# Performance work log

Measured on AMD Instinct MI355X. Metric: run time of the kernel, lower is better.

## Reference

```python
import jax, jax.numpy as jnp
import numpy as np

NBINS = 64
VMIN, VMAX = -3.0, 3.0  # value_range


def setup_inputs() -> dict:
    key = jax.random.key(0)
    x = jax.random.normal(key, (4096, 8192), dtype=jnp.float32)
    return {"x": x}


def reference(x):
    # input_axis = 1 (last axis): per-row fixed-width histogram, normalized by row length.
    B, N = x.shape
    # Bucketize: same semantics as tf.histogram_fixed_width -- scale into [0, nbins),
    # clip out-of-range values into the edge bins.
    scale = NBINS / (VMAX - VMIN)
    bins = jnp.clip(jnp.floor((x - VMIN) * scale).astype(jnp.int32), 0, NBINS - 1)  # [B, N]
    # Fused parallel scatter-add: offset each row into its own bin range.
    row = jnp.arange(B, dtype=jnp.int32)[:, None]               # [B, 1]
    flat_idx = (row * NBINS + bins).reshape(-1)                 # [B*N]
    counts = jax.ops.segment_sum(
        jnp.ones((B * N,), dtype=jnp.float32), flat_idx, num_segments=B * NBINS
    ).reshape(B, NBINS)
    # TF layer returns count / input.shape[input_axis]
    return counts / jnp.float32(N)
```

## Files before the change

### kernel.cpp

```cpp
#include <hip/hip_runtime.h>

#define NBINS 64
#define NCOPIES 64
#define BLOCK 256
#define UNROLL 8

__global__ __launch_bounds__(BLOCK, 8) void hist_rows_kernel(
    const float* __restrict__ x, float* __restrict__ out, int ncols) {
    __shared__ unsigned int hist[NBINS * NCOPIES];

    const int t = threadIdx.x;
    const int row = blockIdx.x;

    #pragma unroll
    for (int i = t; i < NBINS * NCOPIES; i += BLOCK) hist[i] = 0u;
    __syncthreads();

    const int copy = t & (NCOPIES - 1);
    const float vmin = -3.0f;
    const float scale = 64.0f / 6.0f;

    const float4* xr = (const float4*)(x + (size_t)row * (size_t)ncols);
    const int nvec = ncols >> 2;

    int base = 0;
    for (; base + UNROLL * BLOCK <= nvec; base += UNROLL * BLOCK) {
        float4 buf[UNROLL];
        #pragma unroll
        for (int k = 0; k < UNROLL; ++k) buf[k] = xr[base + k * BLOCK + t];
        #pragma unroll
        for (int k = 0; k < UNROLL; ++k) {
            float4 v = buf[k];
            float f0 = __builtin_amdgcn_fmed3f((v.x - vmin) * scale, 0.0f, 63.0f);
            float f1 = __builtin_amdgcn_fmed3f((v.y - vmin) * scale, 0.0f, 63.0f);
            float f2 = __builtin_amdgcn_fmed3f((v.z - vmin) * scale, 0.0f, 63.0f);
            float f3 = __builtin_amdgcn_fmed3f((v.w - vmin) * scale, 0.0f, 63.0f);
            int b0 = (int)f0, b1 = (int)f1, b2 = (int)f2, b3 = (int)f3;
            atomicAdd(&hist[b0 * NCOPIES + copy], 1u);
            atomicAdd(&hist[b1 * NCOPIES + copy], 1u);
            atomicAdd(&hist[b2 * NCOPIES + copy], 1u);
            atomicAdd(&hist[b3 * NCOPIES + copy], 1u);
        }
    }
    for (int i = base + t; i < nvec; i += BLOCK) {
        float4 v = xr[i];
        float f0 = __builtin_amdgcn_fmed3f((v.x - vmin) * scale, 0.0f, 63.0f);
        float f1 = __builtin_amdgcn_fmed3f((v.y - vmin) * scale, 0.0f, 63.0f);
        float f2 = __builtin_amdgcn_fmed3f((v.z - vmin) * scale, 0.0f, 63.0f);
        float f3 = __builtin_amdgcn_fmed3f((v.w - vmin) * scale, 0.0f, 63.0f);
        atomicAdd(&hist[(int)f0 * NCOPIES + copy], 1u);
        atomicAdd(&hist[(int)f1 * NCOPIES + copy], 1u);
        atomicAdd(&hist[(int)f2 * NCOPIES + copy], 1u);
        atomicAdd(&hist[(int)f3 * NCOPIES + copy], 1u);
    }
    __syncthreads();

    if (t < NBINS) {
        unsigned int s = 0;
        #pragma unroll
        for (int c = 0; c < NCOPIES; ++c)
            s += hist[t * NCOPIES + ((c + t) & (NCOPIES - 1))];
        const float inv = 1.0f / (float)ncols;
        out[(size_t)row * NBINS + t] = (float)s * inv;
    }
}

extern "C" void kernel_launch(void* const* d_in, const int* in_sizes, int n_in,
                              void* d_out, int out_size, void* d_ws, size_t ws_size,
                              hipStream_t stream) {
    const float* x = (const float*)d_in[0];
    float* out = (float*)d_out;
    const int nrows = out_size / NBINS;
    const int ncols = in_sizes[0] / nrows;
    hist_rows_kernel<<<nrows, BLOCK, 0, stream>>>(x, out, ncols);
}
```

Before: 184.7 us.

## Specialize single-tile row path, overlap loads with LDS clear, parallelize bin reduction

Adds a fast path for rows of exactly UNROLL*BLOCK float4 (8192 columns) that issues all global loads before zeroing the shared histogram, so memory latency overlaps the clear and barrier. The clear uses 128-bit LDS stores. The final reduction now uses all 256 threads (4 per bin, each summing 16 copies) combined via shuffles instead of 64 threads summing 64 copies. A generic fallback path also handles a scalar tail for column counts not divisible by 4, which the old code silently dropped.

```diff
diff --git a/kernel.cpp b/kernel.cpp
--- a/kernel.cpp
+++ b/kernel.cpp
@@ -11,11 +11,6 @@
 
     const int t = threadIdx.x;
     const int row = blockIdx.x;
-
-    #pragma unroll
-    for (int i = t; i < NBINS * NCOPIES; i += BLOCK) hist[i] = 0u;
-    __syncthreads();
-
     const int copy = t & (NCOPIES - 1);
     const float vmin = -3.0f;
     const float scale = 64.0f / 6.0f;
@@ -23,11 +18,17 @@
     const float4* xr = (const float4*)(x + (size_t)row * (size_t)ncols);
     const int nvec = ncols >> 2;
 
-    int base = 0;
-    for (; base + UNROLL * BLOCK <= nvec; base += UNROLL * BLOCK) {
+    if (nvec == UNROLL * BLOCK) {
         float4 buf[UNROLL];
         #pragma unroll
-        for (int k = 0; k < UNROLL; ++k) buf[k] = xr[base + k * BLOCK + t];
+        for (int k = 0; k < UNROLL; ++k) buf[k] = xr[k * BLOCK + t];
+
+        uint4* h4 = (uint4*)hist;
+        #pragma unroll
+        for (int i = t; i < (NBINS * NCOPIES) / 4; i += BLOCK)
+            h4[i] = make_uint4(0u, 0u, 0u, 0u);
+        __syncthreads();
+
         #pragma unroll
         for (int k = 0; k < UNROLL; ++k) {
             float4 v = buf[k];
@@ -41,27 +42,41 @@
             atomicAdd(&hist[b2 * NCOPIES + copy], 1u);
             atomicAdd(&hist[b3 * NCOPIES + copy], 1u);
         }
-    }
-    for (int i = base + t; i < nvec; i += BLOCK) {
-        float4 v = xr[i];
-        float f0 = __builtin_amdgcn_fmed3f((v.x - vmin) * scale, 0.0f, 63.0f);
-        float f1 = __builtin_amdgcn_fmed3f((v.y - vmin) * scale, 0.0f, 63.0f);
-        float f2 = __builtin_amdgcn_fmed3f((v.z - vmin) * scale, 0.0f, 63.0f);
-        float f3 = __builtin_amdgcn_fmed3f((v.w - vmin) * scale, 0.0f, 63.0f);
-        atomicAdd(&hist[(int)f0 * NCOPIES + copy], 1u);
-        atomicAdd(&hist[(int)f1 * NCOPIES + copy], 1u);
-        atomicAdd(&hist[(int)f2 * NCOPIES + copy], 1u);
-        atomicAdd(&hist[(int)f3 * NCOPIES + copy], 1u);
+    } else {
+        for (int i = t; i < NBINS * NCOPIES; i += BLOCK) hist[i] = 0u;
+        __syncthreads();
+        for (int i = t; i < nvec; i += BLOCK) {
+            float4 v = xr[i];
+            float f0 = __builtin_amdgcn_fmed3f((v.x - vmin) * scale, 0.0f, 63.0f);
+            float f1 = __builtin_amdgcn_fmed3f((v.y - vmin) * scale, 0.0f, 63.0f);
+            float f2 = __builtin_amdgcn_fmed3f((v.z - vmin) * scale, 0.0f, 63.0f);
+            float f3 = __builtin_amdgcn_fmed3f((v.w - vmin) * scale, 0.0f, 63.0f);
+            atomicAdd(&hist[(int)f0 * NCOPIES + copy], 1u);
+            atomicAdd(&hist[(int)f1 * NCOPIES + copy], 1u);
+            atomicAdd(&hist[(int)f2 * NCOPIES + copy], 1u);
+            atomicAdd(&hist[(int)f3 * NCOPIES + copy], 1u);
+        }
+        for (int i = (nvec << 2) + t; i < ncols; i += BLOCK) {
+            float f = __builtin_amdgcn_fmed3f(
+                (x[(size_t)row * (size_t)ncols + i] - vmin) * scale, 0.0f, 63.0f);
+            atomicAdd(&hist[(int)f * NCOPIES + copy], 1u);
+        }
     }
     __syncthreads();
 
-    if (t < NBINS) {
-        unsigned int s = 0;
-        #pragma unroll
-        for (int c = 0; c < NCOPIES; ++c)
-            s += hist[t * NCOPIES + ((c + t) & (NCOPIES - 1))];
+    const int bin = t >> 2;
+    const int part = t & 3;
+    unsigned int s = 0;
+    #pragma unroll
+    for (int j = 0; j < 16; ++j) {
+        const int c = (part * 16 + j + bin) & (NCOPIES - 1);
+        s += hist[bin * NCOPIES + c];
+    }
+    s += __shfl_xor(s, 1);
+    s += __shfl_xor(s, 2);
+    if (part == 0) {
         const float inv = 1.0f / (float)ncols;
-        out[(size_t)row * NBINS + t] = (float)s * inv;
+        out[(size_t)row * NBINS + bin] = (float)s * inv;
     }
 }
 
```

Measured after the change: 184.9 us. Within noise of the previous version (+0.1%).
